# Kernel optimization log

Hardware: AMD Instinct MI355X
Metric: run time of the kernel (lower is better)

The kernel has to match this reference:

```python
import jax, jax.numpy as jnp
import numpy as np

B, N, K = 2, 131072, 9
P, D, S, CI, CO = 4, 4, 1, 8, 8
NH_DIST = 1.0
MIN_SIGMA = 1e-10


def setup_inputs() -> dict:
    key = jax.random.key(0)
    ks = jax.random.split(key, 6)
    x = jax.random.normal(ks[0], (B, N, CI), dtype=jnp.float32)
    # relative cartesian coordinates of each neighbor w.r.t. reference node
    dx = jax.random.normal(ks[1], (B, N, K), dtype=jnp.float32) * 0.5
    dy = jax.random.normal(ks[2], (B, N, K), dtype=jnp.float32) * 0.5
    adj = jax.random.randint(ks[3], (N, K), 0, N, dtype=jnp.int32)
    # fixed polar kernel centers as in __init__
    phis = jnp.linspace(-jnp.pi, jnp.pi, P + 1)[:-1].astype(jnp.float32)
    dists = jnp.linspace(0.0, NH_DIST, D + 2)[1:-1].astype(jnp.float32)
    sigma = jnp.cumsum(jnp.diff(dists))[:S].astype(jnp.float32)
    # amplitudes_no: (n_phi, n_dist, n_sigma, n_amps_in, n_amps_out), xavier-like
    scale = np.sqrt(6.0 / (CI + CO))
    amplitudes_no = jax.random.uniform(ks[4], (P, D, S, CI, CO), dtype=jnp.float32,
                                       minval=-scale, maxval=scale)
    return {"x": x, "dx": dx, "dy": dy, "adj": adj,
            "phis": phis, "dists": dists, "sigma": sigma,
            "amplitudes_no": amplitudes_no}


def reference(x, dx, dy, adj, phis, dists, sigma, amplitudes_no):
    # irregular neighbor gather (get_nh): [B, N, K, CI]
    x_nh = x[:, adj]
    # polar Gaussian kernel centers in cartesian: [P, D]
    mus_lon = jnp.cos(phis)[:, None] * dists[None, :]
    mus_lat = jnp.sin(phis)[:, None] * dists[None, :]
    # offsets: [B, N, K, P, D]
    ddx = dx[..., None, None] - mus_lon
    ddy = dy[..., None, None] - mus_lat
    sig = jnp.clip(sigma, MIN_SIGMA)  # [S]
    r2 = ddx * ddx + ddy * ddy  # [B, N, K, P, D]
    # Gaussian basis weights: [B, N, K, P, D, S]
    w = jnp.exp(-0.5 * r2[..., None] / (sig * sig)) / jnp.sqrt(2.0 * jnp.pi * sig * sig)
    # gather-compute-aggregate: sum over neighbors k and input amplitudes c
    out = jnp.einsum('bnkpds,bnkc,pdsco->bnpdso', w, x_nh, amplitudes_no)
    return out
```

## Files before the change

### kernel.cpp

```cpp
#include <hip/hip_runtime.h>
#include <math.h>

#define N_PTS 131072
#define KNB   9
#define PD    16
#define CIN   8
#define COUT  8
#define PTS_PER_BLK 16
#define THREADS 256
#define AMP_STRIDE 68

typedef float f32x2 __attribute__((ext_vector_type(2)));
typedef float f32x4 __attribute__((ext_vector_type(4)));

#if __has_builtin(__builtin_amdgcn_exp2f)
#define EXP2F(v) __builtin_amdgcn_exp2f(v)
#else
#define EXP2F(v) exp2f(v)
#endif

__global__ __launch_bounds__(THREADS) void polnormal_kernel(
    const float* __restrict__ x,
    const float* __restrict__ dx,
    const float* __restrict__ dy,
    const int*   __restrict__ adj,
    const float* __restrict__ phis,
    const float* __restrict__ dists,
    const float* __restrict__ sigma,
    const float* __restrict__ amp,
    float*       __restrict__ out)
{
    __shared__ float s_dx[PTS_PER_BLK * KNB];
    __shared__ float s_dy[PTS_PER_BLK * KNB];
    __shared__ float s_x[PTS_PER_BLK * KNB * CIN];
    __shared__ float s_amp[PD * AMP_STRIDE];

    const int  tid    = threadIdx.x;
    const long base_g = (long)blockIdx.x * PTS_PER_BLK;
    const int  b      = (int)(base_g >> 17);
    const int  base_n = (int)(base_g & (N_PTS - 1));

    if (tid < 36) {
        ((f32x4*)s_dx)[tid] =
            __builtin_nontemporal_load(&((const f32x4*)dx)[(long)blockIdx.x * 36 + tid]);
    } else if (tid < 72) {
        const int t = tid - 36;
        ((f32x4*)s_dy)[t] =
            __builtin_nontemporal_load(&((const f32x4*)dy)[(long)blockIdx.x * 36 + t]);
    }

    {
        const int pd = tid >> 4;
        const int co = (tid & 15) << 2;
        *(f32x4*)&s_amp[pd * AMP_STRIDE + co] = ((const f32x4*)amp)[tid];
    }

    for (int t = tid; t < PTS_PER_BLK * KNB * 2; t += THREADS) {
        const int  pair = t >> 1;
        const int  half = t & 1;
        const long row  = (long)adj[(long)base_n * KNB + pair];
        const f32x4* src = (const f32x4*)(x + ((long)b * N_PTS + row) * CIN);
        ((f32x4*)s_x)[pair * 2 + half] = src[half];
    }
    __syncthreads();

    const int i  = tid >> 4;
    const int pd = tid & 15;
    const int p  = pd >> 2;
    const int d  = pd & 3;

    const float phi  = phis[p];
    const float dist = dists[d];
    float sn, cs;
    __sincosf(phi, &sn, &cs);
    const float mux = cs * dist;
    const float muy = sn * dist;

    const float sig = fmaxf(sigma[0], 1e-10f);
    const float s2  = sig * sig;
    const float c1 = (-0.5f / s2) * 1.44269504088896340736f;
    const float c2 = -0.5f * __log2f(6.283185307179586f * s2);

    f32x2 wx2[CIN / 2];
#pragma unroll
    for (int c = 0; c < CIN / 2; ++c) wx2[c] = (f32x2)(0.0f);

    const float* sdx = &s_dx[i * KNB];
    const float* sdy = &s_dy[i * KNB];
    const f32x2* sx2 = (const f32x2*)&s_x[i * KNB * CIN];

#pragma unroll
    for (int k = 0; k < KNB; ++k) {
        const float ddx = sdx[k] - mux;
        const float ddy = sdy[k] - muy;
        const float r2  = ddx * ddx + ddy * ddy;
        const float w   = EXP2F(fmaf(r2, c1, c2));
        const f32x2 wv  = (f32x2)(w);
        const f32x2* xr = sx2 + k * (CIN / 2);
#pragma unroll
        for (int c = 0; c < CIN / 2; ++c) wx2[c] += wv * xr[c];
    }

    f32x2 acc2[COUT / 2];
#pragma unroll
    for (int o = 0; o < COUT / 2; ++o) acc2[o] = (f32x2)(0.0f);

    const float* arow = &s_amp[pd * AMP_STRIDE];
#pragma unroll
    for (int c = 0; c < CIN; ++c) {
        const float wc = (c & 1) ? wx2[c >> 1].y : wx2[c >> 1].x;
        const f32x2 wcv = (f32x2)(wc);
        const f32x2* ar = (const f32x2*)(arow + c * COUT);
#pragma unroll
        for (int o = 0; o < COUT / 2; ++o) acc2[o] += wcv * ar[o];
    }

    float* op = out + ((base_g + i) * PD + pd) * COUT;
    f32x4 lo = { acc2[0].x, acc2[0].y, acc2[1].x, acc2[1].y };
    f32x4 hi = { acc2[2].x, acc2[2].y, acc2[3].x, acc2[3].y };
    __builtin_nontemporal_store(lo, (f32x4*)op);
    __builtin_nontemporal_store(hi, (f32x4*)(op + 4));
}

extern "C" void kernel_launch(void* const* d_in, const int* in_sizes, int n_in,
                              void* d_out, int out_size, void* d_ws, size_t ws_size,
                              hipStream_t stream) {
    const float* x     = (const float*)d_in[0];
    const float* dx    = (const float*)d_in[1];
    const float* dy    = (const float*)d_in[2];
    const int*   adj   = (const int*)  d_in[3];
    const float* phis  = (const float*)d_in[4];
    const float* dists = (const float*)d_in[5];
    const float* sigma = (const float*)d_in[6];
    const float* amp   = (const float*)d_in[7];
    float* out = (float*)d_out;

    const int total_pts = 2 * N_PTS;
    const int grid = total_pts / PTS_PER_BLK;
    polnormal_kernel<<<grid, THREADS, 0, stream>>>(x, dx, dy, adj, phis, dists,
                                                   sigma, amp, out);
}
```

Before: 201.2 us.

## Process two points per thread and precompute kernel centers in shared memory

Each block now covers 32 points, with every thread computing two points for the same (p,d) pair so the amplitude row and centre values are reused across both. The dx/dy values are interleaved into a single shared array and read as pairs. The sincos and sigma constants are computed once per block by a few threads instead of per thread. Neighbor rows are gathered as one 32-byte row per thread, and adj is read with nontemporal loads. Doubling the work per thread raises register use and halves the grid size, which can reduce occupancy; the output is memory-bound, so the benefit may be limited.

Measured after the change: 197.3 us. No clear change (-1.9%).

```diff
diff --git a/kernel.cpp b/kernel.cpp
--- a/kernel.cpp
+++ b/kernel.cpp
@@ -6,7 +6,7 @@
 #define PD    16
 #define CIN   8
 #define COUT  8
-#define PTS_PER_BLK 16
+#define PTS_PER_BLK 32
 #define THREADS 256
 #define AMP_STRIDE 68
 
@@ -30,96 +30,120 @@
     const float* __restrict__ amp,
     float*       __restrict__ out)
 {
-    __shared__ float s_dx[PTS_PER_BLK * KNB];
-    __shared__ float s_dy[PTS_PER_BLK * KNB];
+    __shared__ float s_dd[PTS_PER_BLK * KNB * 2];
     __shared__ float s_x[PTS_PER_BLK * KNB * CIN];
     __shared__ float s_amp[PD * AMP_STRIDE];
+    __shared__ float s_mu[2 * PD + 2];
 
     const int  tid    = threadIdx.x;
     const long base_g = (long)blockIdx.x * PTS_PER_BLK;
     const int  b      = (int)(base_g >> 17);
     const int  base_n = (int)(base_g & (N_PTS - 1));
 
-    if (tid < 36) {
-        ((f32x4*)s_dx)[tid] =
-            __builtin_nontemporal_load(&((const f32x4*)dx)[(long)blockIdx.x * 36 + tid]);
-    } else if (tid < 72) {
-        const int t = tid - 36;
-        ((f32x4*)s_dy)[t] =
-            __builtin_nontemporal_load(&((const f32x4*)dy)[(long)blockIdx.x * 36 + t]);
+
+    if (tid < 72) {
+        f32x4 v = __builtin_nontemporal_load(&((const f32x4*)dx)[(long)blockIdx.x * 72 + tid]);
+#pragma unroll
+        for (int j = 0; j < 4; ++j) s_dd[(4 * tid + j) * 2] = v[j];
+    } else if (tid < 144) {
+        const int t = tid - 72;
+        f32x4 v = __builtin_nontemporal_load(&((const f32x4*)dy)[(long)blockIdx.x * 72 + t]);
+#pragma unroll
+        for (int j = 0; j < 4; ++j) s_dd[(4 * t + j) * 2 + 1] = v[j];
+    } else if (tid < 160) {
+        const int pdc = tid - 144;
+        const int p = pdc >> 2, d = pdc & 3;
+        float sn, cs;
+        __sincosf(phis[p], &sn, &cs);
+        const float dist = dists[d];
+        s_mu[pdc * 2]     = cs * dist;
+        s_mu[pdc * 2 + 1] = sn * dist;
+    } else if (tid == 160) {
+        const float sig = fmaxf(sigma[0], 1e-10f);
+        const float s2  = sig * sig;
+        s_mu[32] = (-0.5f / s2) * 1.44269504088896340736f;
+        s_mu[33] = -0.5f * __log2f(6.283185307179586f * s2);
     }
 
     {
-        const int pd = tid >> 4;
-        const int co = (tid & 15) << 2;
-        *(f32x4*)&s_amp[pd * AMP_STRIDE + co] = ((const f32x4*)amp)[tid];
+        const int pdc = tid >> 4;
+        const int co  = (tid & 15) << 2;
+        *(f32x4*)&s_amp[pdc * AMP_STRIDE + co] = ((const f32x4*)amp)[tid];
     }
 
-    for (int t = tid; t < PTS_PER_BLK * KNB * 2; t += THREADS) {
-        const int  pair = t >> 1;
-        const int  half = t & 1;
-        const long row  = (long)adj[(long)base_n * KNB + pair];
+    for (int t = tid; t < PTS_PER_BLK * KNB; t += THREADS) {
+        const long row = (long)__builtin_nontemporal_load(&adj[(long)base_n * KNB + t]);
         const f32x4* src = (const f32x4*)(x + ((long)b * N_PTS + row) * CIN);
-        ((f32x4*)s_x)[pair * 2 + half] = src[half];
+        f32x4* dst = (f32x4*)&s_x[t * CIN];
+        dst[0] = src[0];
+        dst[1] = src[1];
     }
     __syncthreads();
 
     const int i  = tid >> 4;
     const int pd = tid & 15;
-    const int p  = pd >> 2;
-    const int d  = pd & 3;
 
-    const float phi  = phis[p];
-    const float dist = dists[d];
-    float sn, cs;
-    __sincosf(phi, &sn, &cs);
-    const float mux = cs * dist;
-    const float muy = sn * dist;
+    const f32x2 mu  = *(const f32x2*)&s_mu[pd * 2];
+    const float c1  = s_mu[32];
+    const float c2  = s_mu[33];
 
-    const float sig = fmaxf(sigma[0], 1e-10f);
-    const float s2  = sig * sig;
-    const float c1 = (-0.5f / s2) * 1.44269504088896340736f;
-    const float c2 = -0.5f * __log2f(6.283185307179586f * s2);
+    const f32x2* sddA = (const f32x2*)&s_dd[i * KNB * 2];
+    const f32x2* sddB = (const f32x2*)&s_dd[(i + 16) * KNB * 2];
+    const f32x2* sxA  = (const f32x2*)&s_x[i * KNB * CIN];
+    const f32x2* sxB  = (const f32x2*)&s_x[(i + 16) * KNB * CIN];
 
-    f32x2 wx2[CIN / 2];
+    f32x2 wxA[CIN / 2], wxB[CIN / 2];
 #pragma unroll
-    for (int c = 0; c < CIN / 2; ++c) wx2[c] = (f32x2)(0.0f);
-
-    const float* sdx = &s_dx[i * KNB];
-    const float* sdy = &s_dy[i * KNB];
-    const f32x2* sx2 = (const f32x2*)&s_x[i * KNB * CIN];
+    for (int c = 0; c < CIN / 2; ++c) { wxA[c] = (f32x2)(0.0f); wxB[c] = (f32x2)(0.0f); }
 
 #pragma unroll
     for (int k = 0; k < KNB; ++k) {
-        const float ddx = sdx[k] - mux;
-        const float ddy = sdy[k] - muy;
-        const float r2  = ddx * ddx + ddy * ddy;
-        const float w   = EXP2F(fmaf(r2, c1, c2));
-        const f32x2 wv  = (f32x2)(w);
-        const f32x2* xr = sx2 + k * (CIN / 2);
+        const f32x2 ddA = sddA[k];
+        const f32x2 ddB = sddB[k];
+        const float dxA = ddA.x - mu.x, dyA = ddA.y - mu.y;
+        const float dxB = ddB.x - mu.x, dyB = ddB.y - mu.y;
+        const float r2A = dxA * dxA + dyA * dyA;
+        const float r2B = dxB * dxB + dyB * dyB;
+        const float wA  = EXP2F(fmaf(r2A, c1, c2));
+        const float wB  = EXP2F(fmaf(r2B, c1, c2));
+        const f32x2 wvA = (f32x2)(wA), wvB = (f32x2)(wB);
+        const f32x2* xrA = sxA + k * (CIN / 2);
+        const f32x2* xrB = sxB + k * (CIN / 2);
 #pragma unroll
-        for (int c = 0; c < CIN / 2; ++c) wx2[c] += wv * xr[c];
+        for (int c = 0; c < CIN / 2; ++c) {
+            wxA[c] += wvA * xrA[c];
+            wxB[c] += wvB * xrB[c];
+        }
     }
 
-    f32x2 acc2[COUT / 2];
+    f32x2 accA[COUT / 2], accB[COUT / 2];
 #pragma unroll
-    for (int o = 0; o < COUT / 2; ++o) acc2[o] = (f32x2)(0.0f);
+    for (int o = 0; o < COUT / 2; ++o) { accA[o] = (f32x2)(0.0f); accB[o] = (f32x2)(0.0f); }
 
     const float* arow = &s_amp[pd * AMP_STRIDE];
 #pragma unroll
     for (int c = 0; c < CIN; ++c) {
-        const float wc = (c & 1) ? wx2[c >> 1].y : wx2[c >> 1].x;
-        const f32x2 wcv = (f32x2)(wc);
         const f32x2* ar = (const f32x2*)(arow + c * COUT);
+        const float wcA = (c & 1) ? wxA[c >> 1].y : wxA[c >> 1].x;
+        const float wcB = (c & 1) ? wxB[c >> 1].y : wxB[c >> 1].x;
+        const f32x2 wA2 = (f32x2)(wcA), wB2 = (f32x2)(wcB);
 #pragma unroll
-        for (int o = 0; o < COUT / 2; ++o) acc2[o] += wcv * ar[o];
+        for (int o = 0; o < COUT / 2; ++o) {
+            accA[o] += wA2 * ar[o];
+            accB[o] += wB2 * ar[o];
+        }
     }
 
-    float* op = out + ((base_g + i) * PD + pd) * COUT;
-    f32x4 lo = { acc2[0].x, acc2[0].y, acc2[1].x, acc2[1].y };
-    f32x4 hi = { acc2[2].x, acc2[2].y, acc2[3].x, acc2[3].y };
-    __builtin_nontemporal_store(lo, (f32x4*)op);
-    __builtin_nontemporal_store(hi, (f32x4*)(op + 4));
+    float* opA = out + ((base_g + i) * PD + pd) * COUT;
+    float* opB = out + ((base_g + i + 16) * PD + pd) * COUT;
+    f32x4 loA = { accA[0].x, accA[0].y, accA[1].x, accA[1].y };
+    f32x4 hiA = { accA[2].x, accA[2].y, accA[3].x, accA[3].y };
+    f32x4 loB = { accB[0].x, accB[0].y, accB[1].x, accB[1].y };
+    f32x4 hiB = { accB[2].x, accB[2].y, accB[3].x, accB[3].y };
+    __builtin_nontemporal_store(loA, (f32x4*)opA);
+    __builtin_nontemporal_store(hiA, (f32x4*)(opA + 4));
+    __builtin_nontemporal_store(loB, (f32x4*)opB);
+    __builtin_nontemporal_store(hiB, (f32x4*)(opB + 4));
 }
 
 extern "C" void kernel_launch(void* const* d_in, const int* in_sizes, int n_in,
```

## Assign one point per thread and precompute Gaussian exponent terms

Applied to the files above, without the earlier changes.

Restructures the kernel so each thread owns one point and loops over all 16 polar/distance centers, gathering neighbor features directly into registers and staging dx/dy/adj in shared memory. The Gaussian exponent is expanded algebraically so per-neighbor radius terms are computed once and per-center terms are precomputed in shared memory. This removes redundant shared memory traffic and repeated setup, but greatly increases register pressure, reduces the block count, and makes output stores strided per thread.

Measured after the change: 435.0 us. 2.16x slower.

```diff
diff --git a/kernel.cpp b/kernel.cpp
--- a/kernel.cpp
+++ b/kernel.cpp
@@ -6,12 +6,11 @@
 #define PD    16
 #define CIN   8
 #define COUT  8
-#define PTS_PER_BLK 16
 #define THREADS 256
-#define AMP_STRIDE 68
 
 typedef float f32x2 __attribute__((ext_vector_type(2)));
 typedef float f32x4 __attribute__((ext_vector_type(4)));
+typedef int   i32x4 __attribute__((ext_vector_type(4)));
 
 #if __has_builtin(__builtin_amdgcn_exp2f)
 #define EXP2F(v) __builtin_amdgcn_exp2f(v)
@@ -30,96 +29,106 @@
     const float* __restrict__ amp,
     float*       __restrict__ out)
 {
-    __shared__ float s_dx[PTS_PER_BLK * KNB];
-    __shared__ float s_dy[PTS_PER_BLK * KNB];
-    __shared__ float s_x[PTS_PER_BLK * KNB * CIN];
-    __shared__ float s_amp[PD * AMP_STRIDE];
+    __shared__ float s_dd[THREADS * KNB * 2];
+    __shared__ int   s_adj[THREADS * KNB];
+    __shared__ float s_amp[PD * CIN * COUT];
+    __shared__ f32x2 s_t12[PD];
+    __shared__ float s_rr[PD];
+    __shared__ float s_c[2];
 
     const int  tid    = threadIdx.x;
-    const long base_g = (long)blockIdx.x * PTS_PER_BLK;
+    const long base_g = (long)blockIdx.x * THREADS;
     const int  b      = (int)(base_g >> 17);
     const int  base_n = (int)(base_g & (N_PTS - 1));
 
-    if (tid < 36) {
-        ((f32x4*)s_dx)[tid] =
-            __builtin_nontemporal_load(&((const f32x4*)dx)[(long)blockIdx.x * 36 + tid]);
-    } else if (tid < 72) {
-        const int t = tid - 36;
-        ((f32x4*)s_dy)[t] =
-            __builtin_nontemporal_load(&((const f32x4*)dy)[(long)blockIdx.x * 36 + t]);
+
+    for (int t = tid; t < 2 * 576; t += THREADS) {
+        if (t < 576) {
+            f32x4 v = __builtin_nontemporal_load(&((const f32x4*)dx)[(long)blockIdx.x * 576 + t]);
+#pragma unroll
+            for (int j = 0; j < 4; ++j) s_dd[(4 * t + j) * 2] = v[j];
+        } else {
+            const int u = t - 576;
+            f32x4 v = __builtin_nontemporal_load(&((const f32x4*)dy)[(long)blockIdx.x * 576 + u]);
+#pragma unroll
+            for (int j = 0; j < 4; ++j) s_dd[(4 * u + j) * 2 + 1] = v[j];
+        }
     }
+    for (int t = tid; t < 576; t += THREADS) {
+        ((i32x4*)s_adj)[t] =
+            __builtin_nontemporal_load(&((const i32x4*)adj)[((long)base_n * KNB) / 4 + t]);
+    }
+    ((f32x4*)s_amp)[tid] = ((const f32x4*)amp)[tid];
 
-    {
-        const int pd = tid >> 4;
-        const int co = (tid & 15) << 2;
-        *(f32x4*)&s_amp[pd * AMP_STRIDE + co] = ((const f32x4*)amp)[tid];
-    }
-
-    for (int t = tid; t < PTS_PER_BLK * KNB * 2; t += THREADS) {
-        const int  pair = t >> 1;
-        const int  half = t & 1;
-        const long row  = (long)adj[(long)base_n * KNB + pair];
-        const f32x4* src = (const f32x4*)(x + ((long)b * N_PTS + row) * CIN);
-        ((f32x4*)s_x)[pair * 2 + half] = src[half];
+    if (tid < PD) {
+        const float sig = fmaxf(sigma[0], 1e-10f);
+        const float s2  = sig * sig;
+        const float c1  = (-0.5f / s2) * 1.44269504088896340736f;
+        const int p = tid >> 2, d = tid & 3;
+        float sn, cs;
+        __sincosf(phis[p], &sn, &cs);
+        const float dist = dists[d];
+        const float mux = cs * dist, muy = sn * dist;
+        s_t12[tid] = (f32x2){ -2.0f * c1 * mux, -2.0f * c1 * muy };
+        s_rr[tid]  = c1 * (mux * mux + muy * muy);
+        if (tid == 0) {
+            s_c[0] = c1;
+            s_c[1] = -0.5f * __log2f(6.283185307179586f * s2);
+        }
     }
     __syncthreads();
 
-    const int i  = tid >> 4;
-    const int pd = tid & 15;
-    const int p  = pd >> 2;
-    const int d  = pd & 3;
 
-    const float phi  = phis[p];
-    const float dist = dists[d];
-    float sn, cs;
-    __sincosf(phi, &sn, &cs);
-    const float mux = cs * dist;
-    const float muy = sn * dist;
+    f32x2 dd[KNB];
+#pragma unroll
+    for (int k = 0; k < KNB; ++k) dd[k] = *(const f32x2*)&s_dd[(tid * KNB + k) * 2];
 
-    const float sig = fmaxf(sigma[0], 1e-10f);
-    const float s2  = sig * sig;
-    const float c1 = (-0.5f / s2) * 1.44269504088896340736f;
-    const float c2 = -0.5f * __log2f(6.283185307179586f * s2);
-
-    f32x2 wx2[CIN / 2];
-#pragma unroll
-    for (int c = 0; c < CIN / 2; ++c) wx2[c] = (f32x2)(0.0f);
-
-    const float* sdx = &s_dx[i * KNB];
-    const float* sdy = &s_dy[i * KNB];
-    const f32x2* sx2 = (const f32x2*)&s_x[i * KNB * CIN];
-
+    f32x4 xr[KNB][2];
 #pragma unroll
     for (int k = 0; k < KNB; ++k) {
-        const float ddx = sdx[k] - mux;
-        const float ddy = sdy[k] - muy;
-        const float r2  = ddx * ddx + ddy * ddy;
-        const float w   = EXP2F(fmaf(r2, c1, c2));
-        const f32x2 wv  = (f32x2)(w);
-        const f32x2* xr = sx2 + k * (CIN / 2);
-#pragma unroll
-        for (int c = 0; c < CIN / 2; ++c) wx2[c] += wv * xr[c];
+        const long row = (long)s_adj[tid * KNB + k];
+        const f32x4* src = (const f32x4*)(x + (((long)b << 17) + row) * CIN);
+        xr[k][0] = src[0];
+        xr[k][1] = src[1];
     }
 
-    f32x2 acc2[COUT / 2];
+    const float c1 = s_c[0], c2 = s_c[1];
+    float A[KNB];
 #pragma unroll
-    for (int o = 0; o < COUT / 2; ++o) acc2[o] = (f32x2)(0.0f);
-
-    const float* arow = &s_amp[pd * AMP_STRIDE];
-#pragma unroll
-    for (int c = 0; c < CIN; ++c) {
-        const float wc = (c & 1) ? wx2[c >> 1].y : wx2[c >> 1].x;
-        const f32x2 wcv = (f32x2)(wc);
-        const f32x2* ar = (const f32x2*)(arow + c * COUT);
-#pragma unroll
-        for (int o = 0; o < COUT / 2; ++o) acc2[o] += wcv * ar[o];
+    for (int k = 0; k < KNB; ++k) {
+        const float q = fmaf(dd[k].x, dd[k].x, dd[k].y * dd[k].y);
+        A[k] = fmaf(q, c1, c2);
     }
 
-    float* op = out + ((base_g + i) * PD + pd) * COUT;
-    f32x4 lo = { acc2[0].x, acc2[0].y, acc2[1].x, acc2[1].y };
-    f32x4 hi = { acc2[2].x, acc2[2].y, acc2[3].x, acc2[3].y };
-    __builtin_nontemporal_store(lo, (f32x4*)op);
-    __builtin_nontemporal_store(hi, (f32x4*)(op + 4));
+    float* op = out + (long)(base_g + tid) * (PD * COUT);
+
+    for (int pd = 0; pd < PD; ++pd) {
+        const f32x2 t12 = s_t12[pd];
+        const float rr  = s_rr[pd];
+
+        f32x4 wx0 = (f32x4)(0.0f), wx1 = (f32x4)(0.0f);
+#pragma unroll
+        for (int k = 0; k < KNB; ++k) {
+            const float arg = fmaf(t12.x, dd[k].x, fmaf(t12.y, dd[k].y, A[k] + rr));
+            const float w   = EXP2F(arg);
+            const f32x4 wv  = (f32x4)(w);
+            wx0 += wv * xr[k][0];
+            wx1 += wv * xr[k][1];
+        }
+
+        f32x4 acc0 = (f32x4)(0.0f), acc1 = (f32x4)(0.0f);
+        const f32x4* arow = (const f32x4*)&s_amp[pd * (CIN * COUT)];
+#pragma unroll
+        for (int c = 0; c < CIN; ++c) {
+            const float wc  = (c < 4) ? wx0[c] : wx1[c - 4];
+            const f32x4 wcv = (f32x4)(wc);
+            acc0 += wcv * arow[c * 2];
+            acc1 += wcv * arow[c * 2 + 1];
+        }
+
+        __builtin_nontemporal_store(acc0, (f32x4*)(op + pd * 8));
+        __builtin_nontemporal_store(acc1, (f32x4*)(op + pd * 8 + 4));
+    }
 }
 
 extern "C" void kernel_launch(void* const* d_in, const int* in_sizes, int n_in,
@@ -136,7 +145,7 @@
     float* out = (float*)d_out;
 
     const int total_pts = 2 * N_PTS;
-    const int grid = total_pts / PTS_PER_BLK;
+    const int grid = total_pts / THREADS;
     polnormal_kernel<<<grid, THREADS, 0, stream>>>(x, dx, dy, adj, phis, dists,
                                                    sigma, amp, out);
 }
```
